# Kernel optimization log

Measured on AMD Instinct MI355X. Metric: run time of the kernel, lower is better.

Reference implementation:

```python
import jax, jax.numpy as jnp
import numpy as np

B, C, IC, H, W = 16, 256, 128, 32, 32  # batch, in_channels, inter_channels, spatial
EPS = 1e-5


def _conv1x1(x, w, b=None):
    # x: [B,C,H,W], w: [O,C] -> [B,O,H,W]
    y = jnp.einsum('bchw,oc->bohw', x, w)
    if b is not None:
        y = y + b[None, :, None, None]
    return y


def _dot_kernel(x, wt, wp):
    # relu-matmul attention, symmetrized, degree-rsqrt normalized with zero masking
    b, _, h, w = x.shape
    n = h * w
    t = jnp.maximum(_conv1x1(x, wt), 0.0).reshape(b, -1, n)  # [B,IC,N]
    p = jnp.maximum(_conv1x1(x, wp), 0.0).reshape(b, -1, n)  # [B,IC,N]
    att = jnp.einsum('bcn,bcm->bnm', t, p)                    # [B,N,N]
    att = (att + att.transpose(0, 2, 1)) * 0.5
    d = att.sum(axis=2)                                       # [B,N]
    dinv = jnp.where(d != 0, jax.lax.rsqrt(jnp.where(d != 0, d, 1.0)), 0.0)
    return att * dinv[:, None, :] * dinv[:, :, None]


def _bn(x, gamma, beta):
    # BatchNorm2d in training mode (batch statistics, biased variance)
    mu = jnp.mean(x, axis=(0, 2, 3), keepdims=True)
    var = jnp.mean((x - mu) ** 2, axis=(0, 2, 3), keepdims=True)
    xhat = (x - mu) * jax.lax.rsqrt(var + EPS)
    return xhat * gamma[None, :, None, None] + beta[None, :, None, None]


def setup_inputs() -> dict:
    key = jax.random.key(0)
    ks = jax.random.split(key, 32)
    s = 0.05
    inp = {
        'x':  jax.random.normal(ks[0], (B, C, H, W), jnp.float32),
        'ob': jax.random.normal(ks[1], (B, C, H, W), jnp.float32),
        'od': jax.random.normal(ks[2], (B, C, H, W), jnp.float32),
        'Wt': jax.random.normal(ks[3], (IC, C), jnp.float32) * s,
        'Wp': jax.random.normal(ks[4], (IC, C), jnp.float32) * s,
        'Wgx': jax.random.normal(ks[5], (IC, C), jnp.float32) * s,
        'bgx': jax.random.normal(ks[6], (IC,), jnp.float32) * s,
        'Wgb': jax.random.normal(ks[7], (IC, C), jnp.float32) * s,
        'bgb': jax.random.normal(ks[8], (IC,), jnp.float32) * s,
        'Wgd': jax.random.normal(ks[9], (IC, C), jnp.float32) * s,
        'bgd': jax.random.normal(ks[10], (IC,), jnp.float32) * s,
        'Wwx': jax.random.normal(ks[11], (C, IC), jnp.float32) * s,
        'bwx': jax.random.normal(ks[12], (C,), jnp.float32) * s,
        'Wwb': jax.random.normal(ks[13], (C, IC), jnp.float32) * s,
        'bwb': jax.random.normal(ks[14], (C,), jnp.float32) * s,
        'Wwd': jax.random.normal(ks[15], (C, IC), jnp.float32) * s,
        'bwd': jax.random.normal(ks[16], (C,), jnp.float32) * s,
        'Wwxb': jax.random.normal(ks[17], (C, IC), jnp.float32) * s,
        'bwxb': jax.random.normal(ks[18], (C,), jnp.float32) * s,
        'Wwxd': jax.random.normal(ks[19], (C, IC), jnp.float32) * s,
        'bwxd': jax.random.normal(ks[20], (C,), jnp.float32) * s,
        'gamma1': jnp.ones((C,), jnp.float32),
        'beta1': jnp.zeros((C,), jnp.float32),
        'gamma2': jnp.ones((C,), jnp.float32),
        'beta2': jnp.zeros((C,), jnp.float32),
        'Wout': jax.random.normal(ks[21], (C, C), jnp.float32) * s,
        'bout': jax.random.normal(ks[22], (C,), jnp.float32) * s,
    }
    return inp


def reference(x, ob, od, Wt, Wp, Wgx, bgx, Wgb, bgb, Wgd, bgd,
              Wwx, bwx, Wwb, bwb, Wwd, bwd, Wwxb, bwxb, Wwxd, bwxd,
              gamma1, beta1, gamma2, beta2, Wout, bout):
    b, c, h, w = x.shape
    n = h * w

    def g_tokens(inp, wg, bg):
        return _conv1x1(inp, wg, bg).reshape(b, -1, n).transpose(0, 2, 1)  # [B,N,IC]

    g_x = g_tokens(x, Wgx, bgx)
    g_b = g_tokens(ob, Wgb, bgb)
    g_d = g_tokens(od, Wgd, bgd)

    f_x = _dot_kernel(x, Wt, Wp)
    f_b = _dot_kernel(ob, Wt, Wp)
    f_d = _dot_kernel(od, Wt, Wp)

    def agg(f, g):
        # bmm(f,g).transpose(1,2).view(B,IC,H,W)
        return jnp.einsum('bnm,bmi->bin', f, g).reshape(b, -1, h, w)

    x_self = _conv1x1(agg(f_x, g_x), Wwx, bwx)
    ob_self = _conv1x1(agg(f_b, g_b), Wwb, bwb)
    od_self = _conv1x1(agg(f_d, g_d), Wwd, bwd)
    x_ob_cross = _conv1x1(agg(f_b, g_x), Wwxb, bwxb)
    x_od_cross = _conv1x1(agg(f_d, g_x), Wwxd, bwxd)

    od_final = _bn(od_self + x_ob_cross, gamma1, beta1)
    ob_final = _bn(ob_self + x_od_cross, gamma2, beta2)
    output = _conv1x1(od_final + ob_final + x_self, Wout, bout)
    return output + x
```

## Files before the change

### kernel.cpp

```cpp
#include <hip/hip_runtime.h>

#define GAS __attribute__((address_space(1)))
#define LAS __attribute__((address_space(3)))

typedef __attribute__((ext_vector_type(8))) short short8;
typedef __attribute__((ext_vector_type(4))) float f32x4;
typedef unsigned short u16;

constexpr int cB = 16, cC = 256, cIC = 128, cN = 1024;

__device__ __forceinline__ u16 f2bf(float v) {
    unsigned u = __builtin_bit_cast(unsigned, v);
    return (u16)((u + 0x7fffu + ((u >> 16) & 1u)) >> 16);
}
__device__ __forceinline__ float bf2f(u16 v) {
    unsigned u = ((unsigned)v) << 16;
    return __builtin_bit_cast(float, u);
}
__device__ __forceinline__ float rsz(float d) {
    return (d != 0.0f) ? rsqrtf(d) : 0.0f;
}

template<int N> __device__ __forceinline__ void wait_vmcnt() {
    if constexpr (N == 0) asm volatile("s_waitcnt vmcnt(0)" ::: "memory");
    else if constexpr (N == 1) asm volatile("s_waitcnt vmcnt(1)" ::: "memory");
    else if constexpr (N == 2) asm volatile("s_waitcnt vmcnt(2)" ::: "memory");
    else if constexpr (N == 3) asm volatile("s_waitcnt vmcnt(3)" ::: "memory");
    else if constexpr (N == 4) asm volatile("s_waitcnt vmcnt(4)" ::: "memory");
    else if constexpr (N == 5) asm volatile("s_waitcnt vmcnt(5)" ::: "memory");
    else if constexpr (N == 6) asm volatile("s_waitcnt vmcnt(6)" ::: "memory");
    else if constexpr (N == 8) asm volatile("s_waitcnt vmcnt(8)" ::: "memory");
}

template<int BM, int BN, int WR, int WC, bool BREMAP = false>
__device__ __forceinline__ void gemm_core(
    const u16* __restrict__ Ab, const u16* __restrict__ Ab2, int ksplit, int lda,
    const u16* __restrict__ Bb, int ldb, int K,
    u16* lsA, u16* lsB,
    f32x4 (&acc)[BM/(WR*16)][BN/(WC*16)])
{
    constexpr int THREADS = WR * WC * 64;
    constexpr int MR = BM / (WR * 16), NR = BN / (WC * 16);
    constexpr int ACH = (BM * 64) / (THREADS * 16);
    constexpr int BCH = (BN * 64) / (THREADS * 16);
    constexpr int RPC = THREADS / 4;
    constexpr int ISSUES = ACH + BCH;

    const int tid  = threadIdx.x;
    const int lane = tid & 63;
    const int wave = tid >> 6;
    const int wr = wave / WC, wc = wave % WC;
    const int r0 = tid >> 2, slot = tid & 3;

    auto stage = [&](int buf, int kk) {
        const u16* Ak = (Ab2 != nullptr && kk >= ksplit) ? (Ab2 + (kk - ksplit)) : (Ab + kk);
        const u16* Bk = Bb + (BREMAP ? (((kk >> 7) << 8) + (kk & 127)) : kk);
        #pragma unroll
        for (int c = 0; c < ACH; c++) {
            int row = c * RPC + r0;
            int sk = (slot ^ ((row >> 1) & 3)) << 3;
            __builtin_amdgcn_global_load_lds((GAS void*)(Ak + (size_t)row * lda + sk),
                (LAS void*)(lsA + buf * (BM * 32) + c * (THREADS * 8) + (wave << 9)), 16, 0, 0);
        }
        #pragma unroll
        for (int c = 0; c < BCH; c++) {
            int row = c * RPC + r0;
            int sk = (slot ^ ((row >> 1) & 3)) << 3;
            __builtin_amdgcn_global_load_lds((GAS void*)(Bk + (size_t)row * ldb + sk),
                (LAS void*)(lsB + buf * (BN * 32) + c * (THREADS * 8) + (wave << 9)), 16, 0, 0);
        }
    };

    stage(0, 0);
    const int nt = K >> 5;
    for (int t = 0; t < nt; t++) {
        const int cur = t & 1;
        if (t + 1 < nt) { stage(cur ^ 1, (t + 1) << 5); wait_vmcnt<ISSUES>(); }
        else            wait_vmcnt<0>();
        __builtin_amdgcn_s_barrier();
        asm volatile("" ::: "memory");

        const u16* la = lsA + cur * (BM * 32);
        const u16* lb = lsB + cur * (BN * 32);
        short8 af[MR], bf[NR];
        #pragma unroll
        for (int m = 0; m < MR; m++) {
            int row = wr * (BM / WR) + (m << 4) + (lane & 15);
            af[m] = *(const short8*)&la[(row << 5) + (((lane >> 4) ^ ((row >> 1) & 3)) << 3)];
        }
        #pragma unroll
        for (int n = 0; n < NR; n++) {
            int row = wc * (BN / WC) + (n << 4) + (lane & 15);
            bf[n] = *(const short8*)&lb[(row << 5) + (((lane >> 4) ^ ((row >> 1) & 3)) << 3)];
        }
        #pragma unroll
        for (int m = 0; m < MR; m++)
            #pragma unroll
            for (int n = 0; n < NR; n++)
                acc[m][n] = __builtin_amdgcn_mfma_f32_16x16x32_bf16(af[m], bf[n], acc[m][n], 0, 0, 0);

        asm volatile("s_waitcnt lgkmcnt(0)" ::: "memory");
        __builtin_amdgcn_sched_barrier(0);
        __builtin_amdgcn_s_barrier();
    }
}

template<int BM, int BN, int WR, int WC, bool RELU, bool OBF16, bool RBIAS, bool RESID>
__global__ __launch_bounds__(WR*WC*64) void gemm_bt(
    const u16* __restrict__ A, long long sA, long long sA2, int lda,
    const u16* __restrict__ B, long long sB, long long sB2, int ldb,
    void* __restrict__ C, long long sC, long long sC2, int ldc,
    int K,
    const float* __restrict__ bias, int sb2,
    const float* __restrict__ resid, long long sR)
{
    __shared__ alignas(16) u16 lsA[2 * BM * 32];
    __shared__ alignas(16) u16 lsB[2 * BN * 32];

    const int lane = threadIdx.x & 63;
    const int wave = threadIdx.x >> 6;
    const int wr = wave / WC, wc = wave % WC;
    const int zlo = blockIdx.z & 15, zhi = blockIdx.z >> 4;

    const u16* Ab = A + zlo * sA + zhi * sA2 + (size_t)(blockIdx.x * BM) * lda;
    const u16* Bb = B + zlo * sB + zhi * sB2 + (size_t)(blockIdx.y * BN) * ldb;

    f32x4 acc[BM/(WR*16)][BN/(WC*16)] = {};
    gemm_core<BM, BN, WR, WC>(Ab, nullptr, K, lda, Bb, ldb, K, lsA, lsB, acc);

    const int rowb = blockIdx.x * BM + wr * (BM / WR) + ((lane >> 4) << 2);
    const int colb = blockIdx.y * BN + wc * (BN / WC) + (lane & 15);
    const long long cbase = zlo * sC + zhi * sC2;
    #pragma unroll
    for (int m = 0; m < BM/(WR*16); m++) {
        #pragma unroll
        for (int n = 0; n < BN/(WC*16); n++) {
            #pragma unroll
            for (int r = 0; r < 4; r++) {
                int row = rowb + m * 16 + r;
                int col = colb + n * 16;
                float v = acc[m][n][r];
                if (RBIAS) v += bias[zhi * sb2 + row];
                if (RESID) v += resid[zlo * sR + (size_t)row * ldc + col];
                if (RELU)  v = fmaxf(v, 0.0f);
                if (OBF16) ((u16*)C)[cbase + (size_t)row * ldc + col] = f2bf(v);
                else       ((float*)C)[cbase + (size_t)row * ldc + col] = v;
            }
        }
    }
}

__global__ __launch_bounds__(512) void tp_gemm(
    const u16* __restrict__ XT, const u16* __restrict__ WTP,
    u16* __restrict__ TPt, u16* __restrict__ TP, float* __restrict__ CS)
{
    __shared__ alignas(16) u16 lsA[2 * 128 * 32];
    __shared__ alignas(16) u16 lsB[2 * 256 * 32];

    const int id = blockIdx.x;
    const int lane = threadIdx.x & 63;
    const int wave = threadIdx.x >> 6;
    const int wr = wave >> 2, wc = wave & 3;

    if (id < 384) {
        const int z = id >> 3, r_ = id & 7, cx = r_ >> 2, ny = r_ & 3;
        const u16* Ab = WTP + (size_t)(cx * 128) * 256;
        const u16* Bb = XT + (size_t)z * 262144 + (size_t)(ny * 256) * 256;
        f32x4 acc[4][4] = {};
        gemm_core<128, 256, 2, 4>(Ab, nullptr, 256, 256, Bb, 256, 256, lsA, lsB, acc);

        const int rowb = cx * 128 + wr * 64 + ((lane >> 4) << 2);
        const int colb = ny * 256 + wc * 64 + (lane & 15);
        u16* Cb = TPt + (size_t)z * 262144;
        float rp[4][4] = {};
        #pragma unroll
        for (int m = 0; m < 4; m++)
            #pragma unroll
            for (int n = 0; n < 4; n++)
                #pragma unroll
                for (int r = 0; r < 4; r++) {
                    float v = fmaxf(acc[m][n][r], 0.0f);
                    Cb[(size_t)(rowb + m * 16 + r) * 1024 + colb + n * 16] = f2bf(v);
                    rp[m][r] += v;
                }
        #pragma unroll
        for (int m = 0; m < 4; m++)
            #pragma unroll
            for (int r = 0; r < 4; r++) {
                float v = rp[m][r];
                v += __shfl_xor(v, 1, 64);
                v += __shfl_xor(v, 2, 64);
                v += __shfl_xor(v, 4, 64);
                v += __shfl_xor(v, 8, 64);
                if ((lane & 15) == 0)
                    atomicAdd(&CS[z * 256 + rowb + m * 16 + r], v);
            }
    } else {
        const int id2 = id - 384;
        const int z = id2 >> 3, nx = id2 & 7;
        const u16* Ab = XT + (size_t)z * 262144 + (size_t)(nx * 128) * 256;
        f32x4 acc[4][4] = {};
        gemm_core<128, 256, 2, 4>(Ab, nullptr, 256, 256, WTP, 256, 256, lsA, lsB, acc);

        const int rowb = nx * 128 + wr * 64 + ((lane >> 4) << 2);
        const int colb = wc * 64 + (lane & 15);
        u16* Cb = TP + (size_t)z * 262144;
        #pragma unroll
        for (int m = 0; m < 4; m++)
            #pragma unroll
            for (int n = 0; n < 4; n++)
                #pragma unroll
                for (int r = 0; r < 4; r++)
                    Cb[(size_t)(rowb + m * 16 + r) * 256 + colb + n * 16] =
                        f2bf(fmaxf(acc[m][n][r], 0.0f));
    }
}

__global__ __launch_bounds__(256) void g_gemm(
    const u16* __restrict__ XT, const u16* __restrict__ WG,
    const float* __restrict__ BG, const u16* __restrict__ TPt,
    const float* __restrict__ CS, float* __restrict__ DINV,
    u16* __restrict__ GXp, u16* __restrict__ GBp, u16* __restrict__ GDp)
{
    __shared__ alignas(16) u16 lsA[2 * 128 * 32];
    __shared__ alignas(16) u16 lsB[2 * 128 * 32];
    __shared__ float ws[256];
    __shared__ float part[2][128];
    __shared__ float dvs[3][128];

    const int yb = blockIdx.x, zs = blockIdx.z;
    const int stream = zs >> 4, b = zs & 15;
    const int tid = threadIdx.x;

    const int nstr = (stream == 0) ? 3 : 1;
    for (int si = 0; si < nstr; si++) {
        const int s = (stream == 0) ? si : stream;
        const int z2 = s * 16 + b;
        ws[tid] = 0.5f * CS[z2 * 256 + (tid ^ 128)];
        __syncthreads();
        const int col = tid & 127, half = tid >> 7;
        const u16* base = TPt + (size_t)z2 * 262144 + (size_t)(half * 128) * 1024
                        + yb * 128 + col;
        float a = 0;
        #pragma unroll 8
        for (int c = 0; c < 128; c++)
            a += bf2f(base[(size_t)c << 10]) * ws[half * 128 + c];
        part[half][col] = a;
        __syncthreads();
        if (tid < 128) {
            float d = part[0][tid] + part[1][tid];
            if (s == stream) DINV[(zs << 10) + yb * 128 + tid] = d;
            dvs[si][tid] = rsz(d);
        }
        __syncthreads();
    }

    const u16* Ab = WG + stream * 32768;
    const u16* Bb = XT + (size_t)zs * 262144 + (size_t)(yb * 128) * 256;

    f32x4 acc[4][4] = {};
    gemm_core<128, 128, 2, 2>(Ab, nullptr, 256, 256, Bb, 256, 256, lsA, lsB, acc);

    const int lane = threadIdx.x & 63;
    const int wave = threadIdx.x >> 6;
    const int wr = wave >> 1, wc = wave & 1;
    const int rowb = (wr << 6) + ((lane >> 4) << 2);
    const int lcolb = (wc << 6) + (lane & 15);
    const int colb = yb * 128 + lcolb;
    float sx[4], sb_[4], sd[4];
    #pragma unroll
    for (int n = 0; n < 4; n++) {
        int lc = lcolb + n * 16;
        if (stream == 0) { sx[n] = dvs[0][lc]; sb_[n] = dvs[1][lc]; sd[n] = dvs[2][lc]; }
        else if (stream == 1) sb_[n] = dvs[0][lc];
        else sd[n] = dvs[0][lc];
    }
    #pragma unroll
    for (int m = 0; m < 4; m++) {
        #pragma unroll
        for (int r = 0; r < 4; r++) {
            int row = rowb + m * 16 + r;
            float bias = BG[stream * 128 + row];
            #pragma unroll
            for (int n = 0; n < 4; n++) {
                int col = colb + n * 16;
                float v = acc[m][n][r] + bias;
                if (stream == 0) {
                    GXp[(size_t)b * 131072 + ((size_t)row << 10) + col] = f2bf(v * sx[n]);
                    GBp[(size_t)b * 262144 + ((size_t)(row + 128) << 10) + col] = f2bf(v * sb_[n]);
                    GDp[(size_t)b * 262144 + ((size_t)(row + 128) << 10) + col] = f2bf(v * sd[n]);
                } else if (stream == 1) {
                    GBp[(size_t)b * 262144 + ((size_t)row << 10) + col] = f2bf(v * sb_[n]);
                } else {
                    GDp[(size_t)b * 262144 + ((size_t)row << 10) + col] = f2bf(v * sd[n]);
                }
            }
        }
    }
}

__global__ __launch_bounds__(256) void inner_splitk(
    const u16* __restrict__ TPt, const u16* __restrict__ GXp,
    const u16* __restrict__ GBp, const u16* __restrict__ GDp,
    u16* __restrict__ MX, u16* __restrict__ MB, u16* __restrict__ MD)
{
    __shared__ alignas(16) u16 lsA[2 * 128 * 32];
    __shared__ alignas(16) u16 lsB[2 * 128 * 32];

    const int bz = blockIdx.z;
    const int split = bz / 48, z = bz % 48;
    const int which = z >> 4, b = z & 15;
    if (which == 0 && blockIdx.y) return;
    const u16* Gp = (which == 0) ? GXp : (which == 1) ? GBp : GDp;
    u16* M = (which == 0) ? MX : (which == 1) ? MB : MD;
    const int JD  = (which == 0) ? 128 : 256;
    const int ldc = 2 * JD;
    const long long sB = (which == 0) ? 131072 : 262144;

    const u16* Ab = TPt + (size_t)z * 262144 + (size_t)(blockIdx.x * 128) * 1024 + split * 512;
    const u16* Bb = Gp + (size_t)b * sB + (size_t)(blockIdx.y * 128) * 1024 + split * 512;

    f32x4 acc[4][4] = {};
    gemm_core<128, 128, 2, 2>(Ab, nullptr, 512, 1024, Bb, 1024, 512, lsA, lsB, acc);

    const int lane = threadIdx.x & 63;
    const int wave = threadIdx.x >> 6;
    const int wr = wave >> 1, wc = wave & 1;
    const int rowb = blockIdx.x * 128 + (wr << 6) + ((lane >> 4) << 2);
    const int colb = blockIdx.y * 128 + (wc << 6) + (lane & 15);
    u16* Cb = M + (size_t)b * (256 * ldc);
    #pragma unroll
    for (int m = 0; m < 4; m++)
        #pragma unroll
        for (int n = 0; n < 4; n++)
            #pragma unroll
            for (int r = 0; r < 4; r++) {
                int row = (rowb + m * 16 + r) ^ 128;
                int col = split * JD + colb + n * 16;
                Cb[(size_t)row * ldc + col] = f2bf(acc[m][n][r]);
            }
}

__global__ __launch_bounds__(512) void fold_gemm(
    const u16* __restrict__ WF2, const u16* __restrict__ MX,
    const u16* __restrict__ MB, const u16* __restrict__ MD,
    u16* __restrict__ FF2)
{
    __shared__ alignas(16) u16 lsA[2 * 128 * 32];
    __shared__ alignas(16) u16 lsB[2 * 256 * 32];

    const int z = blockIdx.z, q = z >> 4, b = z & 15;
    const int pr = (q == 4) ? 2 : (q >> 1);
    const int side = (q == 1 || q == 3) ? 1 : 0;

    const u16* Ab = WF2 + q * 65536 + (size_t)(blockIdx.x * 128) * 256;

    f32x4 acc[4][4] = {};
    if (q == 4) {
        const u16* Bb = MX + (size_t)b * 65536;
        gemm_core<128, 256, 2, 4, false>(Ab, nullptr, 256, 256, Bb, 256, 256, lsA, lsB, acc);
    } else {
        const u16* Mp = (q == 1 || q == 2) ? MB : MD;
        const int coff = side ? 128 : 0;
        const u16* Bb = Mp + (size_t)b * 131072 + coff;
        gemm_core<128, 256, 2, 4, true>(Ab, nullptr, 256, 256, Bb, 512, 256, lsA, lsB, acc);
    }

    const int lane = threadIdx.x & 63;
    const int wave = threadIdx.x >> 6;
    const int wr = wave >> 2, wc = wave & 3;
    const int rowb = blockIdx.x * 128 + wr * 64 + ((lane >> 4) << 2);
    const int colb = wc * 64 + (lane & 15);
    u16* Cb = FF2 + (size_t)pr * 2097152 + (size_t)b * 131072;
    #pragma unroll
    for (int m = 0; m < 4; m++)
        #pragma unroll
        for (int n = 0; n < 4; n++)
            #pragma unroll
            for (int r = 0; r < 4; r++)
                Cb[(size_t)(rowb + m * 16 + r) * 512 + side * 256 + colb + n * 16]
                    = f2bf(acc[m][n][r]);
}

__global__ __launch_bounds__(512) void outer_gemm(
    const u16* __restrict__ TP, const u16* __restrict__ FF2,
    const float* __restrict__ DINV,
    u16* __restrict__ SALL, float* __restrict__ BNA)
{
    __shared__ alignas(16) u16 lsA[2 * 128 * 32];
    __shared__ alignas(16) u16 lsB[2 * 256 * 32];

    const int z = blockIdx.z, zhi = z >> 4, b = z & 15;
    const int sa1[3] = {2, 1, 0}, sa2[3] = {1, 2, 0};

    const int lane = threadIdx.x & 63;
    const int wave = threadIdx.x >> 6;
    const int wr = wave >> 2, wc = wave & 3;
    const int rowb = blockIdx.x * 128 + wr * 64 + ((lane >> 4) << 2);
    const int colb = wc * 64 + (lane & 15);

    const u16* A1 = TP + (size_t)(sa1[zhi] * 16 + b) * 262144 + (size_t)(blockIdx.x * 128) * 256;
    const u16* B1 = FF2 + (size_t)zhi * 2097152 + (size_t)b * 131072;
    const float* dv1 = DINV + sa1[zhi] * 16384 + (b << 10);

    f32x4 acc[4][4] = {};
    gemm_core<128, 256, 2, 4>(A1, nullptr, 256, 256, B1, 512, 256, lsA, lsB, acc);

    f32x4 keep[4][4];
    #pragma unroll
    for (int m = 0; m < 4; m++) {
        f32x4 dva;
        #pragma unroll
        for (int r = 0; r < 4; r++) dva[r] = rsz(dv1[rowb + m * 16 + r]);
        #pragma unroll
        for (int n = 0; n < 4; n++) keep[m][n] = acc[m][n] * dva;
    }

    if (zhi < 2) {
        const u16* A2 = TP + (size_t)(sa2[zhi] * 16 + b) * 262144 + (size_t)(blockIdx.x * 128) * 256;
        const u16* B2 = B1 + 256;
        const float* dv2 = DINV + sa2[zhi] * 16384 + (b << 10);
        #pragma unroll
        for (int m = 0; m < 4; m++)
            #pragma unroll
            for (int n = 0; n < 4; n++) acc[m][n] = f32x4{0.f, 0.f, 0.f, 0.f};
        gemm_core<128, 256, 2, 4>(A2, nullptr, 256, 256, B2, 512, 256, lsA, lsB, acc);
        #pragma unroll
        for (int m = 0; m < 4; m++) {
            f32x4 dva;
            #pragma unroll
            for (int r = 0; r < 4; r++) dva[r] = rsz(dv2[rowb + m * 16 + r]);
            #pragma unroll
            for (int n = 0; n < 4; n++) keep[m][n] = keep[m][n] + acc[m][n] * dva;
        }
    }

    u16* Cb = SALL + (size_t)b * 786432;
    float csum[4] = {}, csq[4] = {};
    #pragma unroll
    for (int m = 0; m < 4; m++)
        #pragma unroll
        for (int n = 0; n < 4; n++)
            #pragma unroll
            for (int r = 0; r < 4; r++) {
                float v = keep[m][n][r];
                Cb[(size_t)(rowb + m * 16 + r) * 768 + zhi * 256 + colb + n * 16] = f2bf(v);
                csum[n] += v;
                csq[n] += v * v;
            }
    if (zhi < 2) {
        #pragma unroll
        for (int n = 0; n < 4; n++) {
            float s = csum[n], q = csq[n];
            s += __shfl_xor(s, 16, 64); s += __shfl_xor(s, 32, 64);
            q += __shfl_xor(q, 16, 64); q += __shfl_xor(q, 32, 64);
            if (lane < 16) {
                atomicAdd(&BNA[zhi * 512 + colb + n * 16], s);
                atomicAdd(&BNA[zhi * 512 + 256 + colb + n * 16], q);
            }
        }
    }
}

__global__ __launch_bounds__(256) void bnscale(
    const float* __restrict__ Wout, const float* __restrict__ g1, const float* __restrict__ be1,
    const float* __restrict__ g2, const float* __restrict__ be2,
    const float* __restrict__ bwx, const float* __restrict__ bout,
    const float* __restrict__ BNA, u16* __restrict__ WoutS, float* __restrict__ BIAS2)
{
    int o = blockIdx.x, c = threadIdx.x;
    const float inv = 1.0f / 16384.0f;
    float m1 = BNA[c] * inv;
    float v1 = BNA[256 + c] * inv - m1 * m1;
    float sc1 = g1[c] * rsqrtf(v1 + 1e-5f), sh1 = be1[c] - m1 * sc1;
    float m2 = BNA[512 + c] * inv;
    float v2 = BNA[768 + c] * inv - m2 * m2;
    float sc2 = g2[c] * rsqrtf(v2 + 1e-5f), sh2 = be2[c] - m2 * sc2;
    float wv = Wout[o * 256 + c];
    WoutS[o * 768 + c]       = f2bf(wv * sc1);
    WoutS[o * 768 + 256 + c] = f2bf(wv * sc2);
    WoutS[o * 768 + 512 + c] = f2bf(wv);
    __shared__ float red[256];
    red[c] = wv * (sh1 + sh2 + bwx[c]);
    __syncthreads();
    for (int s = 128; s; s >>= 1) { if (c < s) red[c] += red[c + s]; __syncthreads(); }
    if (c == 0) BIAS2[o] = red[0] + bout[o];
}

__global__ __launch_bounds__(256) void prep_transpose(
    const float* __restrict__ x, const float* __restrict__ ob,
    const float* __restrict__ od, u16* __restrict__ xt,
    const float* Wt, const float* Wp,
    const float* Wgx, const float* Wgb, const float* Wgd,
    const float* bgx, const float* bgb, const float* bgd,
    const float* Wwd, const float* Wwxb, const float* Wwb,
    const float* Wwxd, const float* Wwx,
    u16* wtp, u16* wg, u16* wf2, float* bg,
    float* __restrict__ ZZ)
{
    const int tid = threadIdx.x;
    if (blockIdx.z == 48) {
        int base = (blockIdx.y * 16 + blockIdx.x) * 1024;
        #pragma unroll
        for (int l = 0; l < 4; l++) {
            int t = base + l * 256 + tid;
            wtp[t] = f2bf(t < 32768 ? Wt[t] : Wp[t - 32768]);
            if (t < 32768) {
                wg[t] = f2bf(Wgx[t]); wg[32768 + t] = f2bf(Wgb[t]); wg[65536 + t] = f2bf(Wgd[t]);
            }
            {
                int o = t >> 8, k = t & 255, j = k & 127;
                const float* Wq[5] = {Wwd, Wwxb, Wwb, Wwxd, Wwx};
                #pragma unroll
                for (int q = 0; q < 5; q++)
                    wf2[q * 65536 + t] = f2bf(0.5f * Wq[q][o * 128 + j]);
            }
            if (t < 384) bg[t] = (t < 128) ? bgx[t] : (t < 256) ? bgb[t - 128] : bgd[t - 256];
            if (t < 13312) ZZ[t] = 0.0f;
        }
        return;
    }
    __shared__ float ls[64][68];
    const int z = blockIdx.z, which = z >> 4, b = z & 15;
    const float* src = (which == 0) ? x : (which == 1) ? ob : od;
    const float* s = src + (size_t)b * cC * cN;
    u16* dst = xt + (size_t)z * (cN * cC);
    const int n0 = blockIdx.x << 6, c0 = blockIdx.y << 6;

    const int cl0 = tid >> 4, n4 = (tid & 15) << 2;
    #pragma unroll
    for (int p = 0; p < 4; p++) {
        int cl = cl0 + (p << 4);
        f32x4 v = *(const f32x4*)&s[(size_t)(c0 + cl) * cN + n0 + n4];
        ls[cl][n4] = v[0]; ls[cl][n4 + 1] = v[1]; ls[cl][n4 + 2] = v[2]; ls[cl][n4 + 3] = v[3];
    }
    __syncthreads();
    const int nl0 = tid >> 3, c8 = (tid & 7) << 3;
    #pragma unroll
    for (int q = 0; q < 2; q++) {
        int nl = nl0 + (q << 5);
        short8 o;
        #pragma unroll
        for (int j = 0; j < 8; j++) o[j] = (short)f2bf(ls[c8 + j][nl]);
        *(short8*)&dst[(size_t)(n0 + nl) * 256 + c0 + c8] = o;
    }
}

extern "C" void kernel_launch(void* const* d_in, const int* in_sizes, int n_in,
                              void* d_out, int out_size, void* d_ws, size_t ws_size,
                              hipStream_t stream)
{
    const float* x    = (const float*)d_in[0];
    const float* ob   = (const float*)d_in[1];
    const float* od   = (const float*)d_in[2];
    const float* Wt   = (const float*)d_in[3];
    const float* Wp   = (const float*)d_in[4];
    const float* Wgx  = (const float*)d_in[5];
    const float* bgx  = (const float*)d_in[6];
    const float* Wgb  = (const float*)d_in[7];
    const float* bgb  = (const float*)d_in[8];
    const float* Wgd  = (const float*)d_in[9];
    const float* bgd  = (const float*)d_in[10];
    const float* Wwx  = (const float*)d_in[11];
    const float* bwx  = (const float*)d_in[12];
    const float* Wwb  = (const float*)d_in[13];
    const float* Wwd  = (const float*)d_in[15];
    const float* Wwxb = (const float*)d_in[17];
    const float* Wwxd = (const float*)d_in[19];
    const float* g1   = (const float*)d_in[21];
    const float* be1  = (const float*)d_in[22];
    const float* g2   = (const float*)d_in[23];
    const float* be2  = (const float*)d_in[24];
    const float* Wout = (const float*)d_in[25];
    const float* bout = (const float*)d_in[26];
    float* out = (float*)d_out;

    char* w = (char*)d_ws;
    u16*   XT    = (u16*)(w);
    u16*   TPt   = (u16*)(w + 25165824);
    u16*   TP    = (u16*)(w + 50331648);
    u16*   GXp   = (u16*)(w + 75497472);
    u16*   GBp   = (u16*)(w + 79691776);
    u16*   GDp   = (u16*)(w + 88080384);
    u16*   MX    = (u16*)(w + 96468992);
    u16*   MB    = (u16*)(w + 98566144);
    u16*   MD    = (u16*)(w + 102760448);
    u16*   FF2   = (u16*)(w + 106954752);
    u16*   WTP   = (u16*)(w + 119537664);
    u16*   WG    = (u16*)(w + 119668736);
    u16*   WF2   = (u16*)(w + 119865344);
    u16*   WoutS = (u16*)(w + 120520704);
    float* BGf   = (float*)(w + 120913920);
    float* BIAS2 = (float*)(w + 120915968);
    float* DINV  = (float*)(w + 120920064);
    float* ZZ    = (float*)(w + 121116672);

    float* CS   = ZZ;
    float* BNA  = ZZ + 12288;
    u16*   SALL = TPt;

    prep_transpose<<<dim3(16, 4, 49), 256, 0, stream>>>(
        x, ob, od, XT, Wt, Wp, Wgx, Wgb, Wgd, bgx, bgb, bgd,
        Wwd, Wwxb, Wwb, Wwxd, Wwx, WTP, WG, WF2, BGf, ZZ);

    tp_gemm<<<dim3(768), 512, 0, stream>>>(XT, WTP, TPt, TP, CS);

    g_gemm<<<dim3(8, 1, 48), 256, 0, stream>>>(XT, WG, BGf, TPt, CS, DINV,
                                               GXp, GBp, GDp);

    inner_splitk<<<dim3(2, 2, 96), 256, 0, stream>>>(TPt, GXp, GBp, GDp, MX, MB, MD);

    fold_gemm<<<dim3(2, 1, 80), 512, 0, stream>>>(WF2, MX, MB, MD, FF2);

    outer_gemm<<<dim3(8, 1, 48), 512, 0, stream>>>(TP, FF2, DINV, SALL, BNA);

    bnscale<<<dim3(256), 256, 0, stream>>>(Wout, g1, be1, g2, be2, bwx, bout,
                                           BNA, WoutS, BIAS2);

    gemm_bt<128, 128, 2, 2, false, false, true, true><<<dim3(2, 8, 16), 256, 0, stream>>>(
        WoutS, 0, 0, 768,  SALL, 786432, 0, 768,  out, 262144, 0, 1024,
        768, BIAS2, 0, x, 262144);
}
```

Measured before the change: 170.6 us.

## Compute TP once and derive transposed TPt plus degrees via a transpose kernel

The t/p projection GEMM was previously computed twice, once per output layout (TPt and TP), in a 768-block launch. Now only the TP layout is computed, with column sums gathered in the epilogue. A new tiled transpose kernel produces TPt and accumulates the degree vector with atomics during the transpose. The degree dot-product loop is removed from g_gemm, which now reads DINV directly. This halves the projection GEMM work and drops the strided degree reduction, at the cost of an extra kernel launch, an extra read/write pass over TP, and more atomics. The zeroed scratch region is enlarged so it also clears DINV.

Measured after the change: 145.3 us. 1.17x faster.

```diff
diff --git a/kernel.cpp b/kernel.cpp
--- a/kernel.cpp
+++ b/kernel.cpp
@@ -4,6 +4,7 @@
 #define LAS __attribute__((address_space(3)))
 
 typedef __attribute__((ext_vector_type(8))) short short8;
+typedef __attribute__((ext_vector_type(4))) short short4_t;
 typedef __attribute__((ext_vector_type(4))) float f32x4;
 typedef unsigned short u16;
 
@@ -152,108 +153,103 @@
 
 __global__ __launch_bounds__(512) void tp_gemm(
     const u16* __restrict__ XT, const u16* __restrict__ WTP,
-    u16* __restrict__ TPt, u16* __restrict__ TP, float* __restrict__ CS)
+    u16* __restrict__ TP, float* __restrict__ CS)
 {
     __shared__ alignas(16) u16 lsA[2 * 128 * 32];
     __shared__ alignas(16) u16 lsB[2 * 256 * 32];
 
-    const int id = blockIdx.x;
+    const int nx = blockIdx.x, z = blockIdx.z;
+    const u16* Ab = XT + (size_t)z * 262144 + (size_t)(nx * 128) * 256;
+
+    f32x4 acc[4][4] = {};
+    gemm_core<128, 256, 2, 4>(Ab, nullptr, 256, 256, WTP, 256, 256, lsA, lsB, acc);
+
     const int lane = threadIdx.x & 63;
     const int wave = threadIdx.x >> 6;
     const int wr = wave >> 2, wc = wave & 3;
-
-    if (id < 384) {
-        const int z = id >> 3, r_ = id & 7, cx = r_ >> 2, ny = r_ & 3;
-        const u16* Ab = WTP + (size_t)(cx * 128) * 256;
-        const u16* Bb = XT + (size_t)z * 262144 + (size_t)(ny * 256) * 256;
-        f32x4 acc[4][4] = {};
-        gemm_core<128, 256, 2, 4>(Ab, nullptr, 256, 256, Bb, 256, 256, lsA, lsB, acc);
-
-        const int rowb = cx * 128 + wr * 64 + ((lane >> 4) << 2);
-        const int colb = ny * 256 + wc * 64 + (lane & 15);
-        u16* Cb = TPt + (size_t)z * 262144;
-        float rp[4][4] = {};
-        #pragma unroll
-        for (int m = 0; m < 4; m++)
-            #pragma unroll
-            for (int n = 0; n < 4; n++)
-                #pragma unroll
-                for (int r = 0; r < 4; r++) {
-                    float v = fmaxf(acc[m][n][r], 0.0f);
-                    Cb[(size_t)(rowb + m * 16 + r) * 1024 + colb + n * 16] = f2bf(v);
-                    rp[m][r] += v;
-                }
-        #pragma unroll
-        for (int m = 0; m < 4; m++)
+    const int rowb = nx * 128 + wr * 64 + ((lane >> 4) << 2);
+    const int colb = wc * 64 + (lane & 15);
+    u16* Cb = TP + (size_t)z * 262144;
+
+    float cp[4] = {};
+    #pragma unroll
+    for (int m = 0; m < 4; m++)
+        #pragma unroll
+        for (int n = 0; n < 4; n++)
             #pragma unroll
             for (int r = 0; r < 4; r++) {
-                float v = rp[m][r];
-                v += __shfl_xor(v, 1, 64);
-                v += __shfl_xor(v, 2, 64);
-                v += __shfl_xor(v, 4, 64);
-                v += __shfl_xor(v, 8, 64);
-                if ((lane & 15) == 0)
-                    atomicAdd(&CS[z * 256 + rowb + m * 16 + r], v);
-            }
-    } else {
-        const int id2 = id - 384;
-        const int z = id2 >> 3, nx = id2 & 7;
-        const u16* Ab = XT + (size_t)z * 262144 + (size_t)(nx * 128) * 256;
-        f32x4 acc[4][4] = {};
-        gemm_core<128, 256, 2, 4>(Ab, nullptr, 256, 256, WTP, 256, 256, lsA, lsB, acc);
-
-        const int rowb = nx * 128 + wr * 64 + ((lane >> 4) << 2);
-        const int colb = wc * 64 + (lane & 15);
-        u16* Cb = TP + (size_t)z * 262144;
-        #pragma unroll
-        for (int m = 0; m < 4; m++)
-            #pragma unroll
-            for (int n = 0; n < 4; n++)
-                #pragma unroll
-                for (int r = 0; r < 4; r++)
-                    Cb[(size_t)(rowb + m * 16 + r) * 256 + colb + n * 16] =
-                        f2bf(fmaxf(acc[m][n][r], 0.0f));
-    }
+                float v = fmaxf(acc[m][n][r], 0.0f);
+                Cb[(size_t)(rowb + m * 16 + r) * 256 + colb + n * 16] = f2bf(v);
+                cp[n] += v;
+            }
+    #pragma unroll
+    for (int n = 0; n < 4; n++) {
+        float v = cp[n];
+        v += __shfl_xor(v, 16, 64);
+        v += __shfl_xor(v, 32, 64);
+        if (lane < 16)
+            atomicAdd(&CS[z * 256 + colb + n * 16], v);
+    }
+}
+
+__global__ __launch_bounds__(256) void tp_transpose(
+    const u16* __restrict__ TP, const float* __restrict__ CS,
+    u16* __restrict__ TPt, float* __restrict__ DINV)
+{
+    __shared__ u16 ls[64][68];
+    __shared__ float ws[64];
+    __shared__ float pd[4][64];
+
+    const int z = blockIdx.z;
+    const int n0 = blockIdx.x << 6, c0 = blockIdx.y << 6;
+    const int tid = threadIdx.x;
+
+    if (tid < 64) ws[tid] = 0.5f * CS[z * 256 + ((c0 + tid) ^ 128)];
+
+    const u16* src = TP + (size_t)z * 262144;
+    #pragma unroll
+    for (int p = 0; p < 2; p++) {
+        int nl = p * 32 + (tid >> 3);
+        int c8 = (tid & 7) << 3;
+        short8 v = *(const short8*)&src[(size_t)(n0 + nl) * 256 + c0 + c8];
+        #pragma unroll
+        for (int j = 0; j < 8; j++) ls[c8 + j][nl] = (u16)v[j];
+    }
+    __syncthreads();
+
+    u16* dst = TPt + (size_t)z * 262144;
+    #pragma unroll
+    for (int p = 0; p < 2; p++) {
+        int cl = p * 32 + (tid >> 3);
+        int n8 = (tid & 7) << 3;
+        short4_t o0, o1;
+        #pragma unroll
+        for (int j = 0; j < 4; j++) { o0[j] = (short)ls[cl][n8 + j]; o1[j] = (short)ls[cl][n8 + 4 + j]; }
+        *(short4_t*)&dst[(size_t)(c0 + cl) * 1024 + n0 + n8] = o0;
+        *(short4_t*)&dst[(size_t)(c0 + cl) * 1024 + n0 + n8 + 4] = o1;
+    }
+
+    const int n = tid & 63, q = tid >> 6;
+    float a = 0;
+    #pragma unroll
+    for (int c = 0; c < 16; c++) a += bf2f(ls[q * 16 + c][n]) * ws[q * 16 + c];
+    pd[q][n] = a;
+    __syncthreads();
+    if (tid < 64)
+        atomicAdd(&DINV[(z << 10) + n0 + tid],
+                  pd[0][tid] + pd[1][tid] + pd[2][tid] + pd[3][tid]);
 }
 
 __global__ __launch_bounds__(256) void g_gemm(
     const u16* __restrict__ XT, const u16* __restrict__ WG,
-    const float* __restrict__ BG, const u16* __restrict__ TPt,
-    const float* __restrict__ CS, float* __restrict__ DINV,
+    const float* __restrict__ BG, const float* __restrict__ DINV,
     u16* __restrict__ GXp, u16* __restrict__ GBp, u16* __restrict__ GDp)
 {
     __shared__ alignas(16) u16 lsA[2 * 128 * 32];
     __shared__ alignas(16) u16 lsB[2 * 128 * 32];
-    __shared__ float ws[256];
-    __shared__ float part[2][128];
-    __shared__ float dvs[3][128];
 
     const int yb = blockIdx.x, zs = blockIdx.z;
     const int stream = zs >> 4, b = zs & 15;
-    const int tid = threadIdx.x;
-
-    const int nstr = (stream == 0) ? 3 : 1;
-    for (int si = 0; si < nstr; si++) {
-        const int s = (stream == 0) ? si : stream;
-        const int z2 = s * 16 + b;
-        ws[tid] = 0.5f * CS[z2 * 256 + (tid ^ 128)];
-        __syncthreads();
-        const int col = tid & 127, half = tid >> 7;
-        const u16* base = TPt + (size_t)z2 * 262144 + (size_t)(half * 128) * 1024
-                        + yb * 128 + col;
-        float a = 0;
-        #pragma unroll 8
-        for (int c = 0; c < 128; c++)
-            a += bf2f(base[(size_t)c << 10]) * ws[half * 128 + c];
-        part[half][col] = a;
-        __syncthreads();
-        if (tid < 128) {
-            float d = part[0][tid] + part[1][tid];
-            if (s == stream) DINV[(zs << 10) + yb * 128 + tid] = d;
-            dvs[si][tid] = rsz(d);
-        }
-        __syncthreads();
-    }
 
     const u16* Ab = WG + stream * 32768;
     const u16* Bb = XT + (size_t)zs * 262144 + (size_t)(yb * 128) * 256;
@@ -265,15 +261,17 @@
     const int wave = threadIdx.x >> 6;
     const int wr = wave >> 1, wc = wave & 1;
     const int rowb = (wr << 6) + ((lane >> 4) << 2);
-    const int lcolb = (wc << 6) + (lane & 15);
-    const int colb = yb * 128 + lcolb;
+    const int colb = yb * 128 + (wc << 6) + (lane & 15);
+    const float* dvx = DINV + (b << 10);
+    const float* dvb = DINV + 16384 + (b << 10);
+    const float* dvd = DINV + 32768 + (b << 10);
     float sx[4], sb_[4], sd[4];
     #pragma unroll
     for (int n = 0; n < 4; n++) {
-        int lc = lcolb + n * 16;
-        if (stream == 0) { sx[n] = dvs[0][lc]; sb_[n] = dvs[1][lc]; sd[n] = dvs[2][lc]; }
-        else if (stream == 1) sb_[n] = dvs[0][lc];
-        else sd[n] = dvs[0][lc];
+        int col = colb + n * 16;
+        if (stream == 0) { sx[n] = rsz(dvx[col]); sb_[n] = rsz(dvb[col]); sd[n] = rsz(dvd[col]); }
+        else if (stream == 1) sb_[n] = rsz(dvb[col]);
+        else sd[n] = rsz(dvd[col]);
     }
     #pragma unroll
     for (int m = 0; m < 4; m++) {
@@ -516,7 +514,7 @@
                     wf2[q * 65536 + t] = f2bf(0.5f * Wq[q][o * 128 + j]);
             }
             if (t < 384) bg[t] = (t < 128) ? bgx[t] : (t < 256) ? bgb[t - 128] : bgd[t - 256];
-            if (t < 13312) ZZ[t] = 0.0f;
+            if (t < 62464) ZZ[t] = 0.0f;
         }
         return;
     }
@@ -592,21 +590,22 @@
     u16*   WoutS = (u16*)(w + 120520704);
     float* BGf   = (float*)(w + 120913920);
     float* BIAS2 = (float*)(w + 120915968);
-    float* DINV  = (float*)(w + 120920064);
-    float* ZZ    = (float*)(w + 121116672);
+    float* ZZ    = (float*)(w + 120920064);
 
     float* CS   = ZZ;
     float* BNA  = ZZ + 12288;
+    float* DINV = ZZ + 13312;
     u16*   SALL = TPt;
 
     prep_transpose<<<dim3(16, 4, 49), 256, 0, stream>>>(
         x, ob, od, XT, Wt, Wp, Wgx, Wgb, Wgd, bgx, bgb, bgd,
         Wwd, Wwxb, Wwb, Wwxd, Wwx, WTP, WG, WF2, BGf, ZZ);
 
-    tp_gemm<<<dim3(768), 512, 0, stream>>>(XT, WTP, TPt, TP, CS);
-
-    g_gemm<<<dim3(8, 1, 48), 256, 0, stream>>>(XT, WG, BGf, TPt, CS, DINV,
-                                               GXp, GBp, GDp);
+    tp_gemm<<<dim3(8, 1, 48), 512, 0, stream>>>(XT, WTP, TP, CS);
+
+    tp_transpose<<<dim3(16, 4, 48), 256, 0, stream>>>(TP, CS, TPt, DINV);
+
+    g_gemm<<<dim3(8, 1, 48), 256, 0, stream>>>(XT, WG, BGf, DINV, GXp, GBp, GDp);
 
     inner_splitk<<<dim3(2, 2, 96), 256, 0, stream>>>(TPt, GXp, GBp, GDp, MX, MB, MD);
 
```
